# Performance work log

Hardware: AMD Instinct MI355X
Metric: run time of the kernel (lower is better)

The kernel has to match this reference:

```python
import jax, jax.numpy as jnp
import numpy as np

N_NODES = 100000
N_EDGES = 1600000
F_IN = 128
HID = 128  # nhid*2
NHID = 64
N_GRAPHS = 512
N_CLASSES = 10
NEG_SLOPE = 0.2  # PyG GATConv default


def setup_inputs() -> dict:
    key = jax.random.key(0)
    ks = jax.random.split(key, 16)
    x = jax.random.normal(ks[0], (N_NODES, F_IN), dtype=jnp.float32)
    edge_index = jax.random.randint(ks[1], (2, N_EDGES), 0, N_NODES, dtype=jnp.int64)
    batch = jnp.sort(jax.random.randint(ks[2], (N_NODES,), 0, N_GRAPHS, dtype=jnp.int64))
    def lin(k, fan_in, shape):
        bound = 1.0 / np.sqrt(fan_in)
        return jax.random.uniform(k, shape, jnp.float32, -bound, bound)
    return {
        "x": x, "edge_index": edge_index, "batch": batch,
        "W1": lin(ks[3], F_IN, (F_IN, HID)),
        "a_src1": lin(ks[4], HID, (HID,)),
        "a_dst1": lin(ks[5], HID, (HID,)),
        "b1": jnp.zeros((HID,), jnp.float32),
        "W2": lin(ks[6], HID, (HID, HID)),
        "a_src2": lin(ks[7], HID, (HID,)),
        "a_dst2": lin(ks[8], HID, (HID,)),
        "b2": jnp.zeros((HID,), jnp.float32),
        "W_fc1": lin(ks[9], HID, (HID, NHID)),
        "b_fc1": lin(ks[10], HID, (NHID,)),
        "W_fc2": lin(ks[11], NHID, (NHID, N_CLASSES)),
        "b_fc2": lin(ks[12], NHID, (N_CLASSES,)),
    }


def gat_conv(x, src, dst, W, a_src, a_dst, b):
    # h = W x ; attention e_ij = LeakyReLU(a_src.h_i + a_dst.h_j), softmax over
    # incoming edges of each destination j, then scatter-add aggregation.
    h = x @ W                                   # [N, H]
    alpha_s = h @ a_src                         # [N]
    alpha_d = h @ a_dst                         # [N]
    e = jax.nn.leaky_relu(alpha_s[src] + alpha_d[dst], NEG_SLOPE)  # [E]
    n = x.shape[0]
    m = jax.ops.segment_max(e, dst, num_segments=n)                # per-dst max
    ex = jnp.exp(e - m[dst])
    denom = jax.ops.segment_sum(ex, dst, num_segments=n)
    alpha = ex / denom[dst]                                        # [E]
    out = jax.ops.segment_sum(alpha[:, None] * h[src], dst, num_segments=n)
    return out + b


def reference(x, edge_index, batch, W1, a_src1, a_dst1, b1,
              W2, a_src2, a_dst2, b2, W_fc1, b_fc1, W_fc2, b_fc2):
    n = x.shape[0]
    # GATConv default add_self_loops=True
    loops = jnp.arange(n, dtype=edge_index.dtype)
    src = jnp.concatenate([edge_index[0], loops])
    dst = jnp.concatenate([edge_index[1], loops])

    h = jax.nn.selu(gat_conv(x, src, dst, W1, a_src1, a_dst1, b1))
    h = jax.nn.selu(gat_conv(h, src, dst, W2, a_src2, a_dst2, b2))

    # global mean pool over graphs
    sums = jax.ops.segment_sum(h, batch, num_segments=N_GRAPHS)
    cnts = jax.ops.segment_sum(jnp.ones((n,), h.dtype), batch, num_segments=N_GRAPHS)
    pooled = jax.nn.selu(sums / jnp.maximum(cnts, 1.0)[:, None])   # [G, H]

    g = jax.nn.selu(pooled @ W_fc1 + b_fc1)
    # dropout p=0.5 is identity in eval mode
    logits = g @ W_fc2 + b_fc2
    return jax.nn.log_softmax(logits, axis=-1)
```

## Files before the change

kernel.cpp:

```cpp
#include <hip/hip_runtime.h>
#include <hip/hip_bf16.h>

#define NEG_SLOPE 0.2f
typedef unsigned int uint32;

#define BSHIFT 9
#define BSIZE 512
#define MAXB 256
#define PCHUNK 4096

typedef __attribute__((ext_vector_type(8))) __bf16 bf16x8;
typedef __attribute__((ext_vector_type(4))) float f32x4;

__device__ __forceinline__ float selu_f(float x) {
    const float a = 1.6732632423543772f, s = 1.0507009873554805f;
    return x > 0.0f ? s * x : s * a * (__expf(x) - 1.0f);
}

__device__ __forceinline__ unsigned short f2bf(float x) {
    uint32 u = __float_as_uint(x);
    uint32 r = (u + 0x7fff + ((u >> 16) & 1)) >> 16;
    return (unsigned short)r;
}
__device__ __forceinline__ float bf_lo(uint32 g) { return __uint_as_float(g << 16); }
__device__ __forceinline__ float bf_hi(uint32 g) { return __uint_as_float(g & 0xffff0000u); }

__global__ __launch_bounds__(256) void repack_w(const float* __restrict__ W1,
                                                const float* __restrict__ W2,
                                                unsigned short* __restrict__ Wb) {
    const float* W = blockIdx.x ? W2 : W1;
    unsigned short* oh = Wb + (size_t)blockIdx.x * 32768;
    unsigned short* ol = oh + 16384;
    for (int d = threadIdx.x; d < 16384; d += 256) {
        int j = d & 7, nn = (d >> 3) & 127, g = d >> 10;
        float v = W[(g * 8 + j) * 128 + nn];
        uint32 hu = f2bf(v);
        float hv = __uint_as_float(hu << 16);
        oh[d] = (unsigned short)hu;
        ol[d] = f2bf(v - hv);
    }
}

__device__ __forceinline__ void gemm_core(const bf16x8 ah[2][4],
                                          const __bf16* Wl,
                                          const float* a_src, const float* a_dst,
                                          uint32* hb, float* as_, float* ad_,
                                          int rbase, int n, int col16, int quad) {
    f32x4 acc[2][8];
    #pragma unroll
    for (int mt = 0; mt < 2; ++mt)
        #pragma unroll
        for (int t = 0; t < 8; ++t) acc[mt][t] = (f32x4)(0.0f);

    #pragma unroll
    for (int c = 0; c < 4; ++c) {
        #pragma unroll
        for (int t = 0; t < 8; ++t) {
            int off = (((c * 4 + quad) * 128) + t * 16 + col16) * 8;
            bf16x8 bh = *(const bf16x8*)&Wl[off];
            bf16x8 bl = *(const bf16x8*)&Wl[16384 + off];
            #pragma unroll
            for (int mt = 0; mt < 2; ++mt) {
                acc[mt][t] = __builtin_amdgcn_mfma_f32_16x16x32_bf16(ah[mt][c], bh, acc[mt][t], 0, 0, 0);
                acc[mt][t] = __builtin_amdgcn_mfma_f32_16x16x32_bf16(ah[mt][c], bl, acc[mt][t], 0, 0, 0);
            }
        }
    }
    float asv[8], adv[8];
    #pragma unroll
    for (int t = 0; t < 8; ++t) { asv[t] = a_src[t * 16 + col16]; adv[t] = a_dst[t * 16 + col16]; }
    #pragma unroll
    for (int mt = 0; mt < 2; ++mt) {
        #pragma unroll
        for (int reg = 0; reg < 4; ++reg) {
            float s = 0.0f, d = 0.0f;
            #pragma unroll
            for (int t = 0; t < 8; ++t) {
                float v = acc[mt][t][reg];
                s += v * asv[t]; d += v * adv[t];
            }
            #pragma unroll
            for (int off = 1; off < 16; off <<= 1) {
                s += __shfl_xor(s, off);
                d += __shfl_xor(d, off);
            }
            int r = rbase + mt * 16 + quad * 4 + reg;
            if (col16 == 0 && r < n) { as_[r] = s; ad_[r] = d; }
        }
    }
    #pragma unroll
    for (int mt = 0; mt < 2; ++mt)
    #pragma unroll
    for (int t = 0; t < 8; ++t)
    #pragma unroll
    for (int reg = 0; reg < 4; ++reg) {
        float v = acc[mt][t][reg];
        float p = __shfl_xor(v, 1);
        int r = rbase + mt * 16 + quad * 4 + reg;
        if (!(col16 & 1) && r < n) {
            uint32 pk = (uint32)f2bf(v) | ((uint32)f2bf(p) << 16);
            hb[(size_t)r * 64 + t * 8 + (col16 >> 1)] = pk;
        }
    }
}

__global__ __launch_bounds__(256) void gemm_mfma_f32(const float* __restrict__ X,
                                                     const unsigned short* __restrict__ Wbh,
                                                     const float* __restrict__ a_src,
                                                     const float* __restrict__ a_dst,
                                                     uint32* __restrict__ hb,
                                                     float* __restrict__ as_,
                                                     float* __restrict__ ad_, int n) {
    __shared__ __bf16 Wl[32768];
    const int tid = threadIdx.x;
    {
        const uint4* sw = (const uint4*)Wbh;
        uint4* dw = (uint4*)Wl;
        for (int i = tid; i < 4096; i += 256) dw[i] = sw[i];
    }
    const int lane = tid & 63, wid = tid >> 6;
    const int col16 = lane & 15, quad = lane >> 4;
    const int rbase = blockIdx.x * 128 + wid * 32;
    bf16x8 ah[2][4];
    #pragma unroll
    for (int mt = 0; mt < 2; ++mt) {
        int r = rbase + mt * 16 + col16;
        bool ok = (r < n);
        const float* xp = X + (size_t)r * 128;
        #pragma unroll
        for (int c = 0; c < 4; ++c) {
            int k0 = c * 32 + quad * 8;
            float4 x0 = ok ? *(const float4*)(xp + k0)     : make_float4(0.f,0.f,0.f,0.f);
            float4 x1 = ok ? *(const float4*)(xp + k0 + 4) : make_float4(0.f,0.f,0.f,0.f);
            float xs[8] = {x0.x,x0.y,x0.z,x0.w,x1.x,x1.y,x1.z,x1.w};
            #pragma unroll
            for (int j = 0; j < 8; ++j) ah[mt][c][j] = (__bf16)xs[j];
        }
    }
    __syncthreads();
    gemm_core(ah, Wl, a_src, a_dst, hb, as_, ad_, rbase, n, col16, quad);
}

__global__ __launch_bounds__(256) void gemm_mfma_bf16(const __bf16* __restrict__ X,
                                                      const unsigned short* __restrict__ Wbh,
                                                      const float* __restrict__ a_src,
                                                      const float* __restrict__ a_dst,
                                                      uint32* __restrict__ hb,
                                                      float* __restrict__ as_,
                                                      float* __restrict__ ad_, int n) {
    __shared__ __bf16 Wl[32768];
    const int tid = threadIdx.x;
    {
        const uint4* sw = (const uint4*)Wbh;
        uint4* dw = (uint4*)Wl;
        for (int i = tid; i < 4096; i += 256) dw[i] = sw[i];
    }
    const int lane = tid & 63, wid = tid >> 6;
    const int col16 = lane & 15, quad = lane >> 4;
    const int rbase = blockIdx.x * 128 + wid * 32;
    bf16x8 ah[2][4];
    const bf16x8 zz = (bf16x8)((__bf16)0.0f);
    #pragma unroll
    for (int mt = 0; mt < 2; ++mt) {
        int r = rbase + mt * 16 + col16;
        bool ok = (r < n);
        const __bf16* xp = X + (size_t)r * 128;
        #pragma unroll
        for (int c = 0; c < 4; ++c)
            ah[mt][c] = ok ? *(const bf16x8*)(xp + c * 32 + quad * 8) : zz;
    }
    __syncthreads();
    gemm_core(ah, Wl, a_src, a_dst, hb, as_, ad_, rbase, n, col16, quad);
}

__global__ __launch_bounds__(256) void bucket_hist(const int* __restrict__ ei,
                                                   int* __restrict__ gcnt, int E, int TOT) {
    __shared__ int lh[MAXB];
    int t = threadIdx.x;
    lh[t] = 0;
    __syncthreads();
    int eb = blockIdx.x * PCHUNK;
    #pragma unroll
    for (int k = 0; k < PCHUNK / 256; ++k) {
        int e = eb + k * 256 + t;
        if (e < TOT) {
            int d = (e < E) ? ei[E + e] : e - E;
            atomicAdd(&lh[d >> BSHIFT], 1);
        }
    }
    __syncthreads();
    if (lh[t] > 0) atomicAdd(&gcnt[t], lh[t]);
}

__global__ __launch_bounds__(256) void bucket_scan(const int* __restrict__ gcnt,
                                                   int* __restrict__ bstart,
                                                   int* __restrict__ gcursor, int NB, int TOT) {
    __shared__ int sh[256];
    int t = threadIdx.x;
    int v = (t < NB) ? gcnt[t] : 0;
    sh[t] = v;
    __syncthreads();
    for (int off = 1; off < 256; off <<= 1) {
        int add = (t >= off) ? sh[t - off] : 0;
        __syncthreads();
        sh[t] += add;
        __syncthreads();
    }
    int ex = sh[t] - v;
    if (t < NB) { bstart[t] = ex; gcursor[t] = ex; }
    if (t == 0) bstart[NB] = TOT;
}

__global__ __launch_bounds__(256) void partition_edges(const int* __restrict__ ei,
                                                       int* __restrict__ gcursor,
                                                       uint32* __restrict__ tmp,
                                                       int E, int TOT) {
    __shared__ int lcnt[MAXB];
    __shared__ int lstart[MAXB];
    __shared__ int lcur[MAXB];
    __shared__ int gbase[MAXB];
    __shared__ uint32 staged[PCHUNK];
    __shared__ unsigned char bslot[PCHUNK];
    int t = threadIdx.x;
    int eb = blockIdx.x * PCHUNK;
    int sreg[16], dreg[16];
    #pragma unroll
    for (int k = 0; k < 16; ++k) {
        int e = eb + k * 256 + t;
        if (e < TOT) {
            if (e < E) { sreg[k] = ei[e]; dreg[k] = ei[E + e]; }
            else       { sreg[k] = dreg[k] = e - E; }
        } else dreg[k] = -1;
    }
    lcnt[t] = 0;
    __syncthreads();
    #pragma unroll
    for (int k = 0; k < 16; ++k)
        if (dreg[k] >= 0) atomicAdd(&lcnt[dreg[k] >> BSHIFT], 1);
    __syncthreads();
    int v = lcnt[t];
    lstart[t] = v;
    __syncthreads();
    for (int off = 1; off < 256; off <<= 1) {
        int add = (t >= off) ? lstart[t - off] : 0;
        __syncthreads();
        lstart[t] += add;
        __syncthreads();
    }
    int ex = lstart[t] - v;
    __syncthreads();
    lstart[t] = ex;
    lcur[t] = ex;
    if (v > 0) gbase[t] = atomicAdd(&gcursor[t], v);
    __syncthreads();
    #pragma unroll
    for (int k = 0; k < 16; ++k) {
        int d = dreg[k];
        if (d >= 0) {
            int b = d >> BSHIFT;
            int p = atomicAdd(&lcur[b], 1);
            staged[p] = ((uint32)(d & (BSIZE - 1)) << 17) | (uint32)sreg[k];
            bslot[p] = (unsigned char)b;
        }
    }
    __syncthreads();
    int nvalid = TOT - eb; if (nvalid > PCHUNK) nvalid = PCHUNK;
    for (int i = t; i < nvalid; i += 256) {
        int b = bslot[i];
        tmp[gbase[b] + (i - lstart[b])] = staged[i];
    }
}

__global__ __launch_bounds__(256) void bucket_build(const uint32* __restrict__ tmp,
                                                    const int* __restrict__ bstart,
                                                    int* __restrict__ rowptr,
                                                    int* __restrict__ col,
                                                    int N, int TOT, int NB) {
    __shared__ int cnt[BSIZE];
    __shared__ int sums[256];
    int b = blockIdx.x, t = threadIdx.x;
    int lo = b << BSHIFT;
    int nn = N - lo; if (nn > BSIZE) nn = BSIZE;
    cnt[t] = 0; cnt[t + 256] = 0;
    __syncthreads();
    int ebeg = bstart[b], eend = bstart[b + 1];
    for (int i = ebeg + t; i < eend; i += 256)
        atomicAdd(&cnt[tmp[i] >> 17], 1);
    __syncthreads();
    int c0 = cnt[2 * t], c1 = cnt[2 * t + 1];
    int s2 = c0 + c1;
    sums[t] = s2;
    __syncthreads();
    for (int off = 1; off < 256; off <<= 1) {
        int add = (t >= off) ? sums[t - off] : 0;
        __syncthreads();
        sums[t] += add;
        __syncthreads();
    }
    int ex = sums[t] - s2;
    int st0 = ebeg + ex, st1 = st0 + c0;
    if (2 * t < nn)     rowptr[lo + 2 * t] = st0;
    if (2 * t + 1 < nn) rowptr[lo + 2 * t + 1] = st1;
    cnt[2 * t] = st0; cnt[2 * t + 1] = st1;
    __syncthreads();
    for (int i = ebeg + t; i < eend; i += 256) {
        uint32 u = tmp[i];
        int p = atomicAdd(&cnt[u >> 17], 1);
        col[p] = (int)(u & 0x1FFFFu);
    }
    if (b == NB - 1 && t == 0) rowptr[N] = TOT;
}

__global__ __launch_bounds__(256) void gat_csr3(const int* __restrict__ rowptr,
                                                const int* __restrict__ col,
                                                const uint2* __restrict__ hb2,
                                                const float* __restrict__ as_,
                                                const float* __restrict__ ad_,
                                                const float* __restrict__ bias,
                                                uint2* __restrict__ outb, int n) {
    __shared__ float wsh[4][2][32];
    __shared__ int   ssh[4][2][32];
    const int wid = threadIdx.x >> 6;
    const int lane = threadIdx.x & 63;
    const int sub = lane >> 5, l = lane & 31;
    const int node = blockIdx.x * 8 + wid * 2 + sub;
    const bool valid = node < n;
    int beg = 0, end = 0;
    if (valid) { beg = rowptr[node]; end = rowptr[node + 1]; }
    float add = valid ? ad_[node] : 0.0f;
    int deg = end - beg;
    int mdeg = max(deg, __shfl_xor(deg, 32));
    float m = -INFINITY, s = 0.0f;
    float a0 = 0.f, a1 = 0.f, a2 = 0.f, a3 = 0.f;
    for (int cb = 0; cb < mdeg; cb += 32) {
        int j = beg + cb + l;
        bool eok = (j < end);
        int srcn = eok ? col[j] : 0;
        float v = eok ? (as_[srcn] + add) : -INFINITY;
        v = (v > 0.0f) ? v : NEG_SLOPE * v;
        float cm = v;
        #pragma unroll
        for (int off = 16; off > 0; off >>= 1) cm = fmaxf(cm, __shfl_xor(cm, off));
        float nm = fmaxf(m, cm);
        float w = eok ? __expf(v - nm) : 0.0f;
        float ws = w;
        #pragma unroll
        for (int off = 16; off > 0; off >>= 1) ws += __shfl_xor(ws, off);
        float scale = (m == -INFINITY) ? 0.0f : __expf(m - nm);
        s = s * scale + ws;
        a0 *= scale; a1 *= scale; a2 *= scale; a3 *= scale;
        wsh[wid][sub][l] = w;
        ssh[wid][sub][l] = srcn;
        int cnt = end - beg - cb;
        cnt = (cnt > 32) ? 32 : (cnt < 0 ? 0 : cnt);
        int t = 0;
        for (; t + 8 <= cnt; t += 8) {
            int sr[8]; float wr[8]; uint2 g[8];
            #pragma unroll
            for (int q = 0; q < 8; ++q) { sr[q] = ssh[wid][sub][t + q]; wr[q] = wsh[wid][sub][t + q]; }
            #pragma unroll
            for (int q = 0; q < 8; ++q) g[q] = hb2[(uint32)sr[q] * 32u + l];
            #pragma unroll
            for (int q = 0; q < 8; ++q) {
                a0 += wr[q] * bf_lo(g[q].x); a1 += wr[q] * bf_hi(g[q].x);
                a2 += wr[q] * bf_lo(g[q].y); a3 += wr[q] * bf_hi(g[q].y);
            }
        }
        for (; t < cnt; ++t) {
            int sn = ssh[wid][sub][t];
            float wt = wsh[wid][sub][t];
            uint2 g = hb2[(uint32)sn * 32u + l];
            a0 += wt * bf_lo(g.x); a1 += wt * bf_hi(g.x);
            a2 += wt * bf_lo(g.y); a3 += wt * bf_hi(g.y);
        }
        m = nm;
    }
    if (valid) {
        float inv = 1.0f / s;
        float4 bv = *(const float4*)&bias[l * 4];
        float r0 = selu_f(a0 * inv + bv.x);
        float r1 = selu_f(a1 * inv + bv.y);
        float r2 = selu_f(a2 * inv + bv.z);
        float r3 = selu_f(a3 * inv + bv.w);
        uint2 o;
        o.x = (uint32)f2bf(r0) | ((uint32)f2bf(r1) << 16);
        o.y = (uint32)f2bf(r2) | ((uint32)f2bf(r3) << 16);
        outb[(uint32)node * 32u + l] = o;
    }
}

__global__ __launch_bounds__(256) void graph_bounds(const int* __restrict__ batch,
                                                    int* __restrict__ gstart, int n, int G) {
    int i = blockIdx.x * 256 + threadIdx.x;
    if (i >= n) return;
    int b = batch[i];
    int bp = (i == 0) ? -1 : batch[i - 1];
    for (int q = bp + 1; q <= b; ++q) gstart[q] = i;
    if (i == n - 1)
        for (int q = b + 1; q <= G; ++q) gstart[q] = n;
}

__global__ __launch_bounds__(128) void pool_head(const uint32* __restrict__ act,
                                                 const int* __restrict__ gstart,
                                                 const float* __restrict__ Wfc1,
                                                 const float* __restrict__ bfc1,
                                                 const float* __restrict__ Wfc2,
                                                 const float* __restrict__ bfc2,
                                                 float* __restrict__ out) {
    __shared__ float part[128][2];
    __shared__ float p[128];
    __shared__ float q[64];
    __shared__ float l[10];
    __shared__ float red[2];
    int g = blockIdx.x, t = threadIdx.x;
    int lo = gstart[g], hi = gstart[g + 1];
    int half = t >> 6, u = t & 63;
    float acc0 = 0.f, acc1 = 0.f;
    for (int nd = lo + half; nd < hi; nd += 2) {
        uint32 gv = act[(uint32)nd * 64u + u];
        acc0 += bf_lo(gv); acc1 += bf_hi(gv);
    }
    part[t][0] = acc0; part[t][1] = acc1;
    __syncthreads();
    if (half == 0) {
        float c = fmaxf((float)(hi - lo), 1.0f);
        p[2 * u]     = selu_f((acc0 + part[t + 64][0]) / c);
        p[2 * u + 1] = selu_f((acc1 + part[t + 64][1]) / c);
    }
    __syncthreads();
    if (t < 64) {
        float a = bfc1[t];
        #pragma unroll 8
        for (int k = 0; k < 128; ++k) a += p[k] * Wfc1[k * 64 + t];
        q[t] = selu_f(a);
    }
    __syncthreads();
    if (t < 10) {
        float a = bfc2[t];
        #pragma unroll
        for (int k = 0; k < 64; ++k) a += q[k] * Wfc2[k * 10 + t];
        l[t] = a;
    }
    __syncthreads();
    if (t == 0) {
        float mx = l[0];
        for (int c = 1; c < 10; ++c) mx = fmaxf(mx, l[c]);
        float sum = 0.0f;
        for (int c = 0; c < 10; ++c) sum += __expf(l[c] - mx);
        red[0] = mx; red[1] = logf(sum);
    }
    __syncthreads();
    if (t < 10) out[g * 10 + t] = l[t] - red[0] - red[1];
}

extern "C" void kernel_launch(void* const* d_in, const int* in_sizes, int n_in,
                              void* d_out, int out_size, void* d_ws, size_t ws_size,
                              hipStream_t stream) {
    const float* x      = (const float*)d_in[0];
    const int*   ei     = (const int*)d_in[1];
    const int*   batch  = (const int*)d_in[2];
    const float* W1     = (const float*)d_in[3];
    const float* asrc1  = (const float*)d_in[4];
    const float* adst1  = (const float*)d_in[5];
    const float* b1     = (const float*)d_in[6];
    const float* W2     = (const float*)d_in[7];
    const float* asrc2  = (const float*)d_in[8];
    const float* adst2  = (const float*)d_in[9];
    const float* b2     = (const float*)d_in[10];
    const float* Wfc1   = (const float*)d_in[11];
    const float* bfc1   = (const float*)d_in[12];
    const float* Wfc2   = (const float*)d_in[13];
    const float* bfc2   = (const float*)d_in[14];
    float* out = (float*)d_out;

    const int N = in_sizes[0] / 128;
    const int E = in_sizes[1] / 2;
    const int G = out_size / 10;
    const int TOT = E + N;
    const int NB = ((N - 1) >> BSHIFT) + 1;

    uint32* hb    = (uint32*)d_ws;
    uint32* h2b   = hb + (size_t)N * 64;
    uint32* tmp   = h2b + (size_t)N * 64;
    float* as_    = (float*)(tmp + TOT);
    float* ad_    = as_ + N;
    int*   gstart = (int*)(ad_ + N);
    int*   rowptr = gstart + (G + 2);
    int*   gcnt   = rowptr + (N + 2);
    int*   bstart = gcnt + MAXB;
    int*   gcursor= bstart + MAXB + 1;
    int*   col    = gcursor + MAXB;
    unsigned short* Wb = (unsigned short*)(((uintptr_t)(col + TOT) + 255) & ~(uintptr_t)255);

    const int gemmGrid = (N + 127) / 128;
    const int partGrid = (TOT + PCHUNK - 1) / PCHUNK;
    const int gatGrid  = (N + 7) / 8;

    repack_w<<<2, 256, 0, stream>>>(W1, W2, Wb);
    hipMemsetAsync(gcnt, 0, MAXB * 4, stream);
    bucket_hist<<<partGrid, 256, 0, stream>>>(ei, gcnt, E, TOT);
    bucket_scan<<<1, 256, 0, stream>>>(gcnt, bstart, gcursor, NB, TOT);
    partition_edges<<<partGrid, 256, 0, stream>>>(ei, gcursor, tmp, E, TOT);
    bucket_build<<<NB, 256, 0, stream>>>(tmp, bstart, rowptr, col, N, TOT, NB);
    graph_bounds<<<(N + 255) / 256, 256, 0, stream>>>(batch, gstart, N, G);

    gemm_mfma_f32<<<gemmGrid, 256, 0, stream>>>(x, Wb, asrc1, adst1, hb, as_, ad_, N);
    gat_csr3<<<gatGrid, 256, 0, stream>>>(rowptr, col, (const uint2*)hb, as_, ad_, b1, (uint2*)h2b, N);

    gemm_mfma_bf16<<<gemmGrid, 256, 0, stream>>>((const __bf16*)h2b, Wb + 32768, asrc2, adst2, hb, as_, ad_, N);
    gat_csr3<<<gatGrid, 256, 0, stream>>>(rowptr, col, (const uint2*)hb, as_, ad_, b2, (uint2*)h2b, N);

    pool_head<<<G, 128, 0, stream>>>(h2b, gstart, Wfc1, bfc1, Wfc2, bfc2, out);
}
```

Before: 417.8 us.

## Fuse setup kernels and switch GAT aggregation to one wave per node

```diff
diff --git a/kernel.cpp b/kernel.cpp
--- a/kernel.cpp
+++ b/kernel.cpp
@@ -25,20 +25,175 @@
 __device__ __forceinline__ float bf_lo(uint32 g) { return __uint_as_float(g << 16); }
 __device__ __forceinline__ float bf_hi(uint32 g) { return __uint_as_float(g & 0xffff0000u); }
 
-__global__ __launch_bounds__(256) void repack_w(const float* __restrict__ W1,
-                                                const float* __restrict__ W2,
-                                                unsigned short* __restrict__ Wb) {
-    const float* W = blockIdx.x ? W2 : W1;
-    unsigned short* oh = Wb + (size_t)blockIdx.x * 32768;
-    unsigned short* ol = oh + 16384;
-    for (int d = threadIdx.x; d < 16384; d += 256) {
-        int j = d & 7, nn = (d >> 3) & 127, g = d >> 10;
-        float v = W[(g * 8 + j) * 128 + nn];
-        uint32 hu = f2bf(v);
-        float hv = __uint_as_float(hu << 16);
-        oh[d] = (unsigned short)hu;
-        ol[d] = f2bf(v - hv);
-    }
+__global__ __launch_bounds__(256) void prep(const float* __restrict__ W1,
+                                            const float* __restrict__ W2,
+                                            unsigned short* __restrict__ Wb,
+                                            const int* __restrict__ batch,
+                                            int* __restrict__ gstart,
+                                            const int* __restrict__ ei,
+                                            int* __restrict__ gpart,
+                                            int N, int G, int E, int TOT, int GB) {
+    __shared__ int lh[MAXB];
+    int b = blockIdx.x, t = threadIdx.x;
+    if (b < 2) {
+        const float* W = b ? W2 : W1;
+        unsigned short* oh = Wb + (size_t)b * 32768;
+        unsigned short* ol = oh + 16384;
+        for (int d = t; d < 16384; d += 256) {
+            int j = d & 7, nn = (d >> 3) & 127, g = d >> 10;
+            float v = W[(g * 8 + j) * 128 + nn];
+            uint32 hu = f2bf(v);
+            float hv = __uint_as_float(hu << 16);
+            oh[d] = (unsigned short)hu;
+            ol[d] = f2bf(v - hv);
+        }
+    } else if (b < 2 + GB) {
+        int i = (b - 2) * 256 + t;
+        if (i < N) {
+            int bb = batch[i];
+            int bp = (i == 0) ? -1 : batch[i - 1];
+            for (int q = bp + 1; q <= bb; ++q) gstart[q] = i;
+            if (i == N - 1)
+                for (int q = bb + 1; q <= G; ++q) gstart[q] = N;
+        }
+    } else {
+        int hb_ = b - 2 - GB;
+        lh[t] = 0;
+        __syncthreads();
+        int eb = hb_ * PCHUNK;
+        #pragma unroll
+        for (int k = 0; k < PCHUNK / 256; ++k) {
+            int e = eb + k * 256 + t;
+            if (e < TOT) {
+                int d = (e < E) ? ei[E + e] : e - E;
+                atomicAdd(&lh[d >> BSHIFT], 1);
+            }
+        }
+        __syncthreads();
+        gpart[hb_ * MAXB + t] = lh[t];
+    }
+}
+
+__global__ __launch_bounds__(256) void bucket_scan2(const int* __restrict__ gpart,
+                                                    int nparts,
+                                                    int* __restrict__ bstart,
+                                                    int* __restrict__ gcursor,
+                                                    int NB, int TOT) {
+    __shared__ int sh[256];
+    int t = threadIdx.x;
+    int v = 0;
+    for (int p = 0; p < nparts; ++p) v += gpart[p * MAXB + t];
+    sh[t] = v;
+    __syncthreads();
+    for (int off = 1; off < 256; off <<= 1) {
+        int add = (t >= off) ? sh[t - off] : 0;
+        __syncthreads();
+        sh[t] += add;
+        __syncthreads();
+    }
+    int ex = sh[t] - v;
+    if (t < NB) { bstart[t] = ex; gcursor[t] = ex; }
+    if (t == 0) bstart[NB] = TOT;
+}
+
+__global__ __launch_bounds__(256) void partition_edges(const int* __restrict__ ei,
+                                                       int* __restrict__ gcursor,
+                                                       uint32* __restrict__ tmp,
+                                                       int E, int TOT) {
+    __shared__ int lcnt[MAXB];
+    __shared__ int lstart[MAXB];
+    __shared__ int lcur[MAXB];
+    __shared__ int gbase[MAXB];
+    __shared__ uint32 staged[PCHUNK];
+    __shared__ unsigned char bslot[PCHUNK];
+    int t = threadIdx.x;
+    int eb = blockIdx.x * PCHUNK;
+    int sreg[16], dreg[16];
+    #pragma unroll
+    for (int k = 0; k < 16; ++k) {
+        int e = eb + k * 256 + t;
+        if (e < TOT) {
+            if (e < E) { sreg[k] = ei[e]; dreg[k] = ei[E + e]; }
+            else       { sreg[k] = dreg[k] = e - E; }
+        } else dreg[k] = -1;
+    }
+    lcnt[t] = 0;
+    __syncthreads();
+    #pragma unroll
+    for (int k = 0; k < 16; ++k)
+        if (dreg[k] >= 0) atomicAdd(&lcnt[dreg[k] >> BSHIFT], 1);
+    __syncthreads();
+    int v = lcnt[t];
+    lstart[t] = v;
+    __syncthreads();
+    for (int off = 1; off < 256; off <<= 1) {
+        int add = (t >= off) ? lstart[t - off] : 0;
+        __syncthreads();
+        lstart[t] += add;
+        __syncthreads();
+    }
+    int ex = lstart[t] - v;
+    __syncthreads();
+    lstart[t] = ex;
+    lcur[t] = ex;
+    if (v > 0) gbase[t] = atomicAdd(&gcursor[t], v);
+    __syncthreads();
+    #pragma unroll
+    for (int k = 0; k < 16; ++k) {
+        int d = dreg[k];
+        if (d >= 0) {
+            int b = d >> BSHIFT;
+            int p = atomicAdd(&lcur[b], 1);
+            staged[p] = ((uint32)(d & (BSIZE - 1)) << 17) | (uint32)sreg[k];
+            bslot[p] = (unsigned char)b;
+        }
+    }
+    __syncthreads();
+    int nvalid = TOT - eb; if (nvalid > PCHUNK) nvalid = PCHUNK;
+    for (int i = t; i < nvalid; i += 256) {
+        int b = bslot[i];
+        tmp[gbase[b] + (i - lstart[b])] = staged[i];
+    }
+}
+
+__global__ __launch_bounds__(256) void bucket_build(const uint32* __restrict__ tmp,
+                                                    const int* __restrict__ bstart,
+                                                    int* __restrict__ rowptr,
+                                                    int* __restrict__ col,
+                                                    int N, int TOT, int NB) {
+    __shared__ int cnt[BSIZE];
+    __shared__ int sums[256];
+    int b = blockIdx.x, t = threadIdx.x;
+    int lo = b << BSHIFT;
+    int nn = N - lo; if (nn > BSIZE) nn = BSIZE;
+    cnt[t] = 0; cnt[t + 256] = 0;
+    __syncthreads();
+    int ebeg = bstart[b], eend = bstart[b + 1];
+    for (int i = ebeg + t; i < eend; i += 256)
+        atomicAdd(&cnt[tmp[i] >> 17], 1);
+    __syncthreads();
+    int c0 = cnt[2 * t], c1 = cnt[2 * t + 1];
+    int s2 = c0 + c1;
+    sums[t] = s2;
+    __syncthreads();
+    for (int off = 1; off < 256; off <<= 1) {
+        int add = (t >= off) ? sums[t - off] : 0;
+        __syncthreads();
+        sums[t] += add;
+        __syncthreads();
+    }
+    int ex = sums[t] - s2;
+    int st0 = ebeg + ex, st1 = st0 + c0;
+    if (2 * t < nn)     rowptr[lo + 2 * t] = st0;
+    if (2 * t + 1 < nn) rowptr[lo + 2 * t + 1] = st1;
+    cnt[2 * t] = st0; cnt[2 * t + 1] = st1;
+    __syncthreads();
+    for (int i = ebeg + t; i < eend; i += 256) {
+        uint32 u = tmp[i];
+        int p = atomicAdd(&cnt[u >> 17], 1);
+        col[p] = (int)(u & 0x1FFFFu);
+    }
+    if (b == NB - 1 && t == 0) rowptr[N] = TOT;
 }
 
 __device__ __forceinline__ void gemm_core(const bf16x8 ah[2][4],
@@ -173,231 +328,93 @@
     gemm_core(ah, Wl, a_src, a_dst, hb, as_, ad_, rbase, n, col16, quad);
 }
 
-__global__ __launch_bounds__(256) void bucket_hist(const int* __restrict__ ei,
-                                                   int* __restrict__ gcnt, int E, int TOT) {
-    __shared__ int lh[MAXB];
-    int t = threadIdx.x;
-    lh[t] = 0;
-    __syncthreads();
-    int eb = blockIdx.x * PCHUNK;
-    #pragma unroll
-    for (int k = 0; k < PCHUNK / 256; ++k) {
-        int e = eb + k * 256 + t;
-        if (e < TOT) {
-            int d = (e < E) ? ei[E + e] : e - E;
-            atomicAdd(&lh[d >> BSHIFT], 1);
-        }
-    }
-    __syncthreads();
-    if (lh[t] > 0) atomicAdd(&gcnt[t], lh[t]);
-}
-
-__global__ __launch_bounds__(256) void bucket_scan(const int* __restrict__ gcnt,
-                                                   int* __restrict__ bstart,
-                                                   int* __restrict__ gcursor, int NB, int TOT) {
-    __shared__ int sh[256];
-    int t = threadIdx.x;
-    int v = (t < NB) ? gcnt[t] : 0;
-    sh[t] = v;
-    __syncthreads();
-    for (int off = 1; off < 256; off <<= 1) {
-        int add = (t >= off) ? sh[t - off] : 0;
-        __syncthreads();
-        sh[t] += add;
-        __syncthreads();
-    }
-    int ex = sh[t] - v;
-    if (t < NB) { bstart[t] = ex; gcursor[t] = ex; }
-    if (t == 0) bstart[NB] = TOT;
-}
-
-__global__ __launch_bounds__(256) void partition_edges(const int* __restrict__ ei,
-                                                       int* __restrict__ gcursor,
-                                                       uint32* __restrict__ tmp,
-                                                       int E, int TOT) {
-    __shared__ int lcnt[MAXB];
-    __shared__ int lstart[MAXB];
-    __shared__ int lcur[MAXB];
-    __shared__ int gbase[MAXB];
-    __shared__ uint32 staged[PCHUNK];
-    __shared__ unsigned char bslot[PCHUNK];
-    int t = threadIdx.x;
-    int eb = blockIdx.x * PCHUNK;
-    int sreg[16], dreg[16];
-    #pragma unroll
-    for (int k = 0; k < 16; ++k) {
-        int e = eb + k * 256 + t;
-        if (e < TOT) {
-            if (e < E) { sreg[k] = ei[e]; dreg[k] = ei[E + e]; }
-            else       { sreg[k] = dreg[k] = e - E; }
-        } else dreg[k] = -1;
-    }
-    lcnt[t] = 0;
-    __syncthreads();
-    #pragma unroll
-    for (int k = 0; k < 16; ++k)
-        if (dreg[k] >= 0) atomicAdd(&lcnt[dreg[k] >> BSHIFT], 1);
-    __syncthreads();
-    int v = lcnt[t];
-    lstart[t] = v;
-    __syncthreads();
-    for (int off = 1; off < 256; off <<= 1) {
-        int add = (t >= off) ? lstart[t - off] : 0;
-        __syncthreads();
-        lstart[t] += add;
-        __syncthreads();
-    }
-    int ex = lstart[t] - v;
-    __syncthreads();
-    lstart[t] = ex;
-    lcur[t] = ex;
-    if (v > 0) gbase[t] = atomicAdd(&gcursor[t], v);
-    __syncthreads();
-    #pragma unroll
-    for (int k = 0; k < 16; ++k) {
-        int d = dreg[k];
-        if (d >= 0) {
-            int b = d >> BSHIFT;
-            int p = atomicAdd(&lcur[b], 1);
-            staged[p] = ((uint32)(d & (BSIZE - 1)) << 17) | (uint32)sreg[k];
-            bslot[p] = (unsigned char)b;
-        }
-    }
-    __syncthreads();
-    int nvalid = TOT - eb; if (nvalid > PCHUNK) nvalid = PCHUNK;
-    for (int i = t; i < nvalid; i += 256) {
-        int b = bslot[i];
-        tmp[gbase[b] + (i - lstart[b])] = staged[i];
-    }
-}
-
-__global__ __launch_bounds__(256) void bucket_build(const uint32* __restrict__ tmp,
-                                                    const int* __restrict__ bstart,
-                                                    int* __restrict__ rowptr,
-                                                    int* __restrict__ col,
-                                                    int N, int TOT, int NB) {
-    __shared__ int cnt[BSIZE];
-    __shared__ int sums[256];
-    int b = blockIdx.x, t = threadIdx.x;
-    int lo = b << BSHIFT;
-    int nn = N - lo; if (nn > BSIZE) nn = BSIZE;
-    cnt[t] = 0; cnt[t + 256] = 0;
-    __syncthreads();
-    int ebeg = bstart[b], eend = bstart[b + 1];
-    for (int i = ebeg + t; i < eend; i += 256)
-        atomicAdd(&cnt[tmp[i] >> 17], 1);
-    __syncthreads();
-    int c0 = cnt[2 * t], c1 = cnt[2 * t + 1];
-    int s2 = c0 + c1;
-    sums[t] = s2;
-    __syncthreads();
-    for (int off = 1; off < 256; off <<= 1) {
-        int add = (t >= off) ? sums[t - off] : 0;
-        __syncthreads();
-        sums[t] += add;
-        __syncthreads();
-    }
-    int ex = sums[t] - s2;
-    int st0 = ebeg + ex, st1 = st0 + c0;
-    if (2 * t < nn)     rowptr[lo + 2 * t] = st0;
-    if (2 * t + 1 < nn) rowptr[lo + 2 * t + 1] = st1;
-    cnt[2 * t] = st0; cnt[2 * t + 1] = st1;
-    __syncthreads();
-    for (int i = ebeg + t; i < eend; i += 256) {
-        uint32 u = tmp[i];
-        int p = atomicAdd(&cnt[u >> 17], 1);
-        col[p] = (int)(u & 0x1FFFFu);
-    }
-    if (b == NB - 1 && t == 0) rowptr[N] = TOT;
-}
-
-__global__ __launch_bounds__(256) void gat_csr3(const int* __restrict__ rowptr,
+__global__ __launch_bounds__(256) void gat_csr4(const int* __restrict__ rowptr,
                                                 const int* __restrict__ col,
-                                                const uint2* __restrict__ hb2,
+                                                const uint4* __restrict__ hb4,
                                                 const float* __restrict__ as_,
                                                 const float* __restrict__ ad_,
                                                 const float* __restrict__ bias,
-                                                uint2* __restrict__ outb, int n) {
-    __shared__ float wsh[4][2][32];
-    __shared__ int   ssh[4][2][32];
+                                                uint4* __restrict__ outb4, int n) {
     const int wid = threadIdx.x >> 6;
     const int lane = threadIdx.x & 63;
-    const int sub = lane >> 5, l = lane & 31;
-    const int node = blockIdx.x * 8 + wid * 2 + sub;
-    const bool valid = node < n;
-    int beg = 0, end = 0;
-    if (valid) { beg = rowptr[node]; end = rowptr[node + 1]; }
-    float add = valid ? ad_[node] : 0.0f;
-    int deg = end - beg;
-    int mdeg = max(deg, __shfl_xor(deg, 32));
+    const int grp = lane >> 4, fl = lane & 15;
+    const int node = blockIdx.x * 4 + wid;
+    if (node >= n) return;
+    const int beg = rowptr[node], end = rowptr[node + 1];
+    const float add = ad_[node];
+    const int deg = end - beg;
     float m = -INFINITY, s = 0.0f;
-    float a0 = 0.f, a1 = 0.f, a2 = 0.f, a3 = 0.f;
-    for (int cb = 0; cb < mdeg; cb += 32) {
-        int j = beg + cb + l;
+    float a0=0.f,a1=0.f,a2=0.f,a3=0.f,a4=0.f,a5=0.f,a6=0.f,a7=0.f;
+    for (int cb = 0; cb < deg; cb += 64) {
+        int j = beg + cb + lane;
         bool eok = (j < end);
         int srcn = eok ? col[j] : 0;
         float v = eok ? (as_[srcn] + add) : -INFINITY;
         v = (v > 0.0f) ? v : NEG_SLOPE * v;
         float cm = v;
         #pragma unroll
-        for (int off = 16; off > 0; off >>= 1) cm = fmaxf(cm, __shfl_xor(cm, off));
+        for (int off = 32; off > 0; off >>= 1) cm = fmaxf(cm, __shfl_xor(cm, off));
         float nm = fmaxf(m, cm);
         float w = eok ? __expf(v - nm) : 0.0f;
         float ws = w;
         #pragma unroll
-        for (int off = 16; off > 0; off >>= 1) ws += __shfl_xor(ws, off);
+        for (int off = 32; off > 0; off >>= 1) ws += __shfl_xor(ws, off);
         float scale = (m == -INFINITY) ? 0.0f : __expf(m - nm);
         s = s * scale + ws;
-        a0 *= scale; a1 *= scale; a2 *= scale; a3 *= scale;
-        wsh[wid][sub][l] = w;
-        ssh[wid][sub][l] = srcn;
-        int cnt = end - beg - cb;
-        cnt = (cnt > 32) ? 32 : (cnt < 0 ? 0 : cnt);
-        int t = 0;
-        for (; t + 8 <= cnt; t += 8) {
-            int sr[8]; float wr[8]; uint2 g[8];
-            #pragma unroll
-            for (int q = 0; q < 8; ++q) { sr[q] = ssh[wid][sub][t + q]; wr[q] = wsh[wid][sub][t + q]; }
-            #pragma unroll
-            for (int q = 0; q < 8; ++q) g[q] = hb2[(uint32)sr[q] * 32u + l];
-            #pragma unroll
-            for (int q = 0; q < 8; ++q) {
-                a0 += wr[q] * bf_lo(g[q].x); a1 += wr[q] * bf_hi(g[q].x);
-                a2 += wr[q] * bf_lo(g[q].y); a3 += wr[q] * bf_hi(g[q].y);
+        a0*=scale; a1*=scale; a2*=scale; a3*=scale;
+        a4*=scale; a5*=scale; a6*=scale; a7*=scale;
+        int cnt = end - beg - cb; cnt = (cnt > 64) ? 64 : cnt;
+        for (int tt = 0; tt < cnt; tt += 8) {
+            int e0 = tt + grp, e1 = tt + 4 + grp;
+            float w0 = __shfl(w, e0);
+            int   s0 = __shfl(srcn, e0);
+            float w1 = __shfl(w, e1);
+            int   s1 = __shfl(srcn, e1);
+            bool v0 = e0 < cnt, v1 = e1 < cnt;
+            uint4 g0, g1;
+            if (v0) g0 = hb4[(uint32)s0 * 16u + fl];
+            if (v1) g1 = hb4[(uint32)s1 * 16u + fl];
+            if (v0) {
+                a0 += w0 * bf_lo(g0.x); a1 += w0 * bf_hi(g0.x);
+                a2 += w0 * bf_lo(g0.y); a3 += w0 * bf_hi(g0.y);
+                a4 += w0 * bf_lo(g0.z); a5 += w0 * bf_hi(g0.z);
+                a6 += w0 * bf_lo(g0.w); a7 += w0 * bf_hi(g0.w);
             }
-        }
-        for (; t < cnt; ++t) {
-            int sn = ssh[wid][sub][t];
-            float wt = wsh[wid][sub][t];
-            uint2 g = hb2[(uint32)sn * 32u + l];
-            a0 += wt * bf_lo(g.x); a1 += wt * bf_hi(g.x);
-            a2 += wt * bf_lo(g.y); a3 += wt * bf_hi(g.y);
+            if (v1) {
+                a0 += w1 * bf_lo(g1.x); a1 += w1 * bf_hi(g1.x);
+                a2 += w1 * bf_lo(g1.y); a3 += w1 * bf_hi(g1.y);
+                a4 += w1 * bf_lo(g1.z); a5 += w1 * bf_hi(g1.z);
+                a6 += w1 * bf_lo(g1.w); a7 += w1 * bf_hi(g1.w);
+            }
         }
         m = nm;
     }
-    if (valid) {
+    #pragma unroll
+    for (int off = 16; off < 64; off <<= 1) {
+        a0 += __shfl_xor(a0, off); a1 += __shfl_xor(a1, off);
+        a2 += __shfl_xor(a2, off); a3 += __shfl_xor(a3, off);
+        a4 += __shfl_xor(a4, off); a5 += __shfl_xor(a5, off);
+        a6 += __shfl_xor(a6, off); a7 += __shfl_xor(a7, off);
+    }
+    if (grp == 0) {
         float inv = 1.0f / s;
-        float4 bv = *(const float4*)&bias[l * 4];
-        float r0 = selu_f(a0 * inv + bv.x);
-        float r1 = selu_f(a1 * inv + bv.y);
-        float r2 = selu_f(a2 * inv + bv.z);
-        float r3 = selu_f(a3 * inv + bv.w);
-        uint2 o;
+        float4 b0 = *(const float4*)&bias[fl * 8];
+        float4 b1 = *(const float4*)&bias[fl * 8 + 4];
+        float r0 = selu_f(a0 * inv + b0.x);
+        float r1 = selu_f(a1 * inv + b0.y);
+        float r2 = selu_f(a2 * inv + b0.z);
+        float r3 = selu_f(a3 * inv + b0.w);
+        float r4 = selu_f(a4 * inv + b1.x);
+        float r5 = selu_f(a5 * inv + b1.y);
+        float r6 = selu_f(a6 * inv + b1.z);
+        float r7 = selu_f(a7 * inv + b1.w);
+        uint4 o;
         o.x = (uint32)f2bf(r0) | ((uint32)f2bf(r1) << 16);
         o.y = (uint32)f2bf(r2) | ((uint32)f2bf(r3) << 16);
-        outb[(uint32)node * 32u + l] = o;
-    }
-}
-
-__global__ __launch_bounds__(256) void graph_bounds(const int* __restrict__ batch,
-                                                    int* __restrict__ gstart, int n, int G) {
-    int i = blockIdx.x * 256 + threadIdx.x;
-    if (i >= n) return;
-    int b = batch[i];
-    int bp = (i == 0) ? -1 : batch[i - 1];
-    for (int q = bp + 1; q <= b; ++q) gstart[q] = i;
-    if (i == n - 1)
-        for (int q = b + 1; q <= G; ++q) gstart[q] = n;
+        o.z = (uint32)f2bf(r4) | ((uint32)f2bf(r5) << 16);
+        o.w = (uint32)f2bf(r6) | ((uint32)f2bf(r7) << 16);
+        outb4[(uint32)node * 16u + fl] = o;
+    }
 }
 
 __global__ __launch_bounds__(128) void pool_head(const uint32* __restrict__ act,
@@ -478,6 +495,8 @@
     const int G = out_size / 10;
     const int TOT = E + N;
     const int NB = ((N - 1) >> BSHIFT) + 1;
+    const int GB = (N + 255) / 256;
+    const int PH = (TOT + PCHUNK - 1) / PCHUNK;
 
     uint32* hb    = (uint32*)d_ws;
     uint32* h2b   = hb + (size_t)N * 64;
@@ -486,29 +505,25 @@
     float* ad_    = as_ + N;
     int*   gstart = (int*)(ad_ + N);
     int*   rowptr = gstart + (G + 2);
-    int*   gcnt   = rowptr + (N + 2);
-    int*   bstart = gcnt + MAXB;
+    int*   bstart = rowptr + (N + 2);
     int*   gcursor= bstart + MAXB + 1;
-    int*   col    = gcursor + MAXB;
+    int*   gpart  = gcursor + MAXB;
+    int*   col    = gpart + PH * MAXB;
     unsigned short* Wb = (unsigned short*)(((uintptr_t)(col + TOT) + 255) & ~(uintptr_t)255);
 
     const int gemmGrid = (N + 127) / 128;
-    const int partGrid = (TOT + PCHUNK - 1) / PCHUNK;
-    const int gatGrid  = (N + 7) / 8;
-
-    repack_w<<<2, 256, 0, stream>>>(W1, W2, Wb);
-    hipMemsetAsync(gcnt, 0, MAXB * 4, stream);
-    bucket_hist<<<partGrid, 256, 0, stream>>>(ei, gcnt, E, TOT);
-    bucket_scan<<<1, 256, 0, stream>>>(gcnt, bstart, gcursor, NB, TOT);
-    partition_edges<<<partGrid, 256, 0, stream>>>(ei, gcursor, tmp, E, TOT);
+    const int gatGrid  = (N + 3) / 4;
+
+    prep<<<2 + GB + PH, 256, 0, stream>>>(W1, W2, Wb, batch, gstart, ei, gpart, N, G, E, TOT, GB);
+    bucket_scan2<<<1, 256, 0, stream>>>(gpart, PH, bstart, gcursor, NB, TOT);
+    partition_edges<<<PH, 256, 0, stream>>>(ei, gcursor, tmp, E, TOT);
     bucket_build<<<NB, 256, 0, stream>>>(tmp, bstart, rowptr, col, N, TOT, NB);
-    graph_bounds<<<(N + 255) / 256, 256, 0, stream>>>(batch, gstart, N, G);
 
     gemm_mfma_f32<<<gemmGrid, 256, 0, stream>>>(x, Wb, asrc1, adst1, hb, as_, ad_, N);
-    gat_csr3<<<gatGrid, 256, 0, stream>>>(rowptr, col, (const uint2*)hb, as_, ad_, b1, (uint2*)h2b, N);
+    gat_csr4<<<gatGrid, 256, 0, stream>>>(rowptr, col, (const uint4*)hb, as_, ad_, b1, (uint4*)h2b, N);
 
     gemm_mfma_bf16<<<gemmGrid, 256, 0, stream>>>((const __bf16*)h2b, Wb + 32768, asrc2, adst2, hb, as_, ad_, N);
-    gat_csr3<<<gatGrid, 256, 0, stream>>>(rowptr, col, (const uint2*)hb, as_, ad_, b2, (uint2*)h2b, N);
+    gat_csr4<<<gatGrid, 256, 0, stream>>>(rowptr, col, (const uint4*)hb, as_, ad_, b2, (uint4*)h2b, N);
 
     pool_head<<<G, 128, 0, stream>>>(h2b, gstart, Wfc1, bfc1, Wfc2, bfc2, out);
 }
```

Measured after the change: 468.2 us. 12.1% more time.

## Merge CSR preprocessing into fused prep kernel with per-chunk local partitions

Applied to the files above, without the earlier changes.

```diff
diff --git a/kernel.cpp b/kernel.cpp
--- a/kernel.cpp
+++ b/kernel.cpp
@@ -25,20 +25,160 @@
 __device__ __forceinline__ float bf_lo(uint32 g) { return __uint_as_float(g << 16); }
 __device__ __forceinline__ float bf_hi(uint32 g) { return __uint_as_float(g & 0xffff0000u); }
 
-__global__ __launch_bounds__(256) void repack_w(const float* __restrict__ W1,
-                                                const float* __restrict__ W2,
-                                                unsigned short* __restrict__ Wb) {
-    const float* W = blockIdx.x ? W2 : W1;
-    unsigned short* oh = Wb + (size_t)blockIdx.x * 32768;
-    unsigned short* ol = oh + 16384;
-    for (int d = threadIdx.x; d < 16384; d += 256) {
-        int j = d & 7, nn = (d >> 3) & 127, g = d >> 10;
-        float v = W[(g * 8 + j) * 128 + nn];
-        uint32 hu = f2bf(v);
-        float hv = __uint_as_float(hu << 16);
-        oh[d] = (unsigned short)hu;
-        ol[d] = f2bf(v - hv);
-    }
+__global__ __launch_bounds__(256) void prep(const float* __restrict__ W1,
+                                            const float* __restrict__ W2,
+                                            unsigned short* __restrict__ Wb,
+                                            const int* __restrict__ batch,
+                                            int* __restrict__ gstart,
+                                            const int* __restrict__ ei,
+                                            uint32* __restrict__ tmp,
+                                            int* __restrict__ cntp,
+                                            int* __restrict__ offp,
+                                            int N, int G, int E, int TOT, int GB) {
+    __shared__ uint32 staged[PCHUNK];
+    __shared__ int lcnt[MAXB];
+    __shared__ int lstart[MAXB];
+    __shared__ int lcur[MAXB];
+    int b = blockIdx.x, t = threadIdx.x;
+    if (b < 2) {
+        const float* W = b ? W2 : W1;
+        unsigned short* oh = Wb + (size_t)b * 32768;
+        unsigned short* ol = oh + 16384;
+        for (int d = t; d < 16384; d += 256) {
+            int j = d & 7, nn = (d >> 3) & 127, g = d >> 10;
+            float v = W[(g * 8 + j) * 128 + nn];
+            uint32 hu = f2bf(v);
+            float hv = __uint_as_float(hu << 16);
+            oh[d] = (unsigned short)hu;
+            ol[d] = f2bf(v - hv);
+        }
+    } else if (b < 2 + GB) {
+        int i = (b - 2) * 256 + t;
+        if (i < N) {
+            int bb = batch[i];
+            int bp = (i == 0) ? -1 : batch[i - 1];
+            for (int q = bp + 1; q <= bb; ++q) gstart[q] = i;
+            if (i == N - 1)
+                for (int q = bb + 1; q <= G; ++q) gstart[q] = N;
+        }
+    } else {
+        int c = b - 2 - GB;
+        int eb = c * PCHUNK;
+        int sreg[16], dreg[16];
+        #pragma unroll
+        for (int k = 0; k < 16; ++k) {
+            int e = eb + k * 256 + t;
+            if (e < TOT) {
+                if (e < E) { sreg[k] = ei[e]; dreg[k] = ei[E + e]; }
+                else       { sreg[k] = dreg[k] = e - E; }
+            } else dreg[k] = -1;
+        }
+        lcnt[t] = 0;
+        __syncthreads();
+        #pragma unroll
+        for (int k = 0; k < 16; ++k)
+            if (dreg[k] >= 0) atomicAdd(&lcnt[dreg[k] >> BSHIFT], 1);
+        __syncthreads();
+        int v = lcnt[t];
+        lstart[t] = v;
+        __syncthreads();
+        for (int off = 1; off < 256; off <<= 1) {
+            int add = (t >= off) ? lstart[t - off] : 0;
+            __syncthreads();
+            lstart[t] += add;
+            __syncthreads();
+        }
+        int ex = lstart[t] - v;
+        cntp[c * MAXB + t] = v;
+        offp[c * MAXB + t] = ex;
+        __syncthreads();
+        lstart[t] = ex;
+        lcur[t] = ex;
+        __syncthreads();
+        #pragma unroll
+        for (int k = 0; k < 16; ++k) {
+            int d = dreg[k];
+            if (d >= 0) {
+                int p = atomicAdd(&lcur[d >> BSHIFT], 1);
+                staged[p] = ((uint32)(d & (BSIZE - 1)) << 17) | (uint32)sreg[k];
+            }
+        }
+        __syncthreads();
+        int nvalid = TOT - eb; if (nvalid > PCHUNK) nvalid = PCHUNK;
+        for (int i = t; i < nvalid; i += 256)
+            tmp[eb + i] = staged[i];
+    }
+}
+
+__global__ __launch_bounds__(256) void scan3(const int* __restrict__ cntp,
+                                             int nchunks,
+                                             int* __restrict__ bstart,
+                                             int NB, int TOT) {
+    __shared__ int sh[256];
+    int t = threadIdx.x;
+    int v = 0;
+    for (int c = 0; c < nchunks; ++c) v += cntp[c * MAXB + t];
+    sh[t] = v;
+    __syncthreads();
+    for (int off = 1; off < 256; off <<= 1) {
+        int add = (t >= off) ? sh[t - off] : 0;
+        __syncthreads();
+        sh[t] += add;
+        __syncthreads();
+    }
+    int ex = sh[t] - v;
+    if (t < NB) bstart[t] = ex;
+    if (t == 0) bstart[NB] = TOT;
+}
+
+__global__ __launch_bounds__(256) void bucket_build2(const uint32* __restrict__ tmp,
+                                                     const int* __restrict__ cntp,
+                                                     const int* __restrict__ offp,
+                                                     const int* __restrict__ bstart,
+                                                     int* __restrict__ rowptr,
+                                                     int* __restrict__ col,
+                                                     int N, int TOT, int NB, int PH) {
+    __shared__ int cnt[BSIZE];
+    __shared__ int sums[256];
+    int b = blockIdx.x, t = threadIdx.x;
+    int lo = b << BSHIFT;
+    int nn = N - lo; if (nn > BSIZE) nn = BSIZE;
+    cnt[t] = 0; cnt[t + 256] = 0;
+    __syncthreads();
+    for (int c = t; c < PH; c += 256) {
+        int cc = cntp[c * MAXB + b];
+        int oo = c * PCHUNK + offp[c * MAXB + b];
+        for (int i = 0; i < cc; ++i)
+            atomicAdd(&cnt[tmp[oo + i] >> 17], 1);
+    }
+    __syncthreads();
+    int c0 = cnt[2 * t], c1 = cnt[2 * t + 1];
+    int s2 = c0 + c1;
+    sums[t] = s2;
+    __syncthreads();
+    for (int off = 1; off < 256; off <<= 1) {
+        int add = (t >= off) ? sums[t - off] : 0;
+        __syncthreads();
+        sums[t] += add;
+        __syncthreads();
+    }
+    int ebeg = bstart[b];
+    int ex = sums[t] - s2;
+    int st0 = ebeg + ex, st1 = st0 + c0;
+    if (2 * t < nn)     rowptr[lo + 2 * t] = st0;
+    if (2 * t + 1 < nn) rowptr[lo + 2 * t + 1] = st1;
+    cnt[2 * t] = st0; cnt[2 * t + 1] = st1;
+    __syncthreads();
+    for (int c = t; c < PH; c += 256) {
+        int cc = cntp[c * MAXB + b];
+        int oo = c * PCHUNK + offp[c * MAXB + b];
+        for (int i = 0; i < cc; ++i) {
+            uint32 u = tmp[oo + i];
+            int p = atomicAdd(&cnt[u >> 17], 1);
+            col[p] = (int)(u & 0x1FFFFu);
+        }
+    }
+    if (b == NB - 1 && t == 0) rowptr[N] = TOT;
 }
 
 __device__ __forceinline__ void gemm_core(const bf16x8 ah[2][4],
@@ -171,144 +311,6 @@
     }
     __syncthreads();
     gemm_core(ah, Wl, a_src, a_dst, hb, as_, ad_, rbase, n, col16, quad);
-}
-
-__global__ __launch_bounds__(256) void bucket_hist(const int* __restrict__ ei,
-                                                   int* __restrict__ gcnt, int E, int TOT) {
-    __shared__ int lh[MAXB];
-    int t = threadIdx.x;
-    lh[t] = 0;
-    __syncthreads();
-    int eb = blockIdx.x * PCHUNK;
-    #pragma unroll
-    for (int k = 0; k < PCHUNK / 256; ++k) {
-        int e = eb + k * 256 + t;
-        if (e < TOT) {
-            int d = (e < E) ? ei[E + e] : e - E;
-            atomicAdd(&lh[d >> BSHIFT], 1);
-        }
-    }
-    __syncthreads();
-    if (lh[t] > 0) atomicAdd(&gcnt[t], lh[t]);
-}
-
-__global__ __launch_bounds__(256) void bucket_scan(const int* __restrict__ gcnt,
-                                                   int* __restrict__ bstart,
-                                                   int* __restrict__ gcursor, int NB, int TOT) {
-    __shared__ int sh[256];
-    int t = threadIdx.x;
-    int v = (t < NB) ? gcnt[t] : 0;
-    sh[t] = v;
-    __syncthreads();
-    for (int off = 1; off < 256; off <<= 1) {
-        int add = (t >= off) ? sh[t - off] : 0;
-        __syncthreads();
-        sh[t] += add;
-        __syncthreads();
-    }
-    int ex = sh[t] - v;
-    if (t < NB) { bstart[t] = ex; gcursor[t] = ex; }
-    if (t == 0) bstart[NB] = TOT;
-}
-
-__global__ __launch_bounds__(256) void partition_edges(const int* __restrict__ ei,
-                                                       int* __restrict__ gcursor,
-                                                       uint32* __restrict__ tmp,
-                                                       int E, int TOT) {
-    __shared__ int lcnt[MAXB];
-    __shared__ int lstart[MAXB];
-    __shared__ int lcur[MAXB];
-    __shared__ int gbase[MAXB];
-    __shared__ uint32 staged[PCHUNK];
-    __shared__ unsigned char bslot[PCHUNK];
-    int t = threadIdx.x;
-    int eb = blockIdx.x * PCHUNK;
-    int sreg[16], dreg[16];
-    #pragma unroll
-    for (int k = 0; k < 16; ++k) {
-        int e = eb + k * 256 + t;
-        if (e < TOT) {
-            if (e < E) { sreg[k] = ei[e]; dreg[k] = ei[E + e]; }
-            else       { sreg[k] = dreg[k] = e - E; }
-        } else dreg[k] = -1;
-    }
-    lcnt[t] = 0;
-    __syncthreads();
-    #pragma unroll
-    for (int k = 0; k < 16; ++k)
-        if (dreg[k] >= 0) atomicAdd(&lcnt[dreg[k] >> BSHIFT], 1);
-    __syncthreads();
-    int v = lcnt[t];
-    lstart[t] = v;
-    __syncthreads();
-    for (int off = 1; off < 256; off <<= 1) {
-        int add = (t >= off) ? lstart[t - off] : 0;
-        __syncthreads();
-        lstart[t] += add;
-        __syncthreads();
-    }
-    int ex = lstart[t] - v;
-    __syncthreads();
-    lstart[t] = ex;
-    lcur[t] = ex;
-    if (v > 0) gbase[t] = atomicAdd(&gcursor[t], v);
-    __syncthreads();
-    #pragma unroll
-    for (int k = 0; k < 16; ++k) {
-        int d = dreg[k];
-        if (d >= 0) {
-            int b = d >> BSHIFT;
-            int p = atomicAdd(&lcur[b], 1);
-            staged[p] = ((uint32)(d & (BSIZE - 1)) << 17) | (uint32)sreg[k];
-            bslot[p] = (unsigned char)b;
-        }
-    }
-    __syncthreads();
-    int nvalid = TOT - eb; if (nvalid > PCHUNK) nvalid = PCHUNK;
-    for (int i = t; i < nvalid; i += 256) {
-        int b = bslot[i];
-        tmp[gbase[b] + (i - lstart[b])] = staged[i];
-    }
-}
-
-__global__ __launch_bounds__(256) void bucket_build(const uint32* __restrict__ tmp,
-                                                    const int* __restrict__ bstart,
-                                                    int* __restrict__ rowptr,
-                                                    int* __restrict__ col,
-                                                    int N, int TOT, int NB) {
-    __shared__ int cnt[BSIZE];
-    __shared__ int sums[256];
-    int b = blockIdx.x, t = threadIdx.x;
-    int lo = b << BSHIFT;
-    int nn = N - lo; if (nn > BSIZE) nn = BSIZE;
-    cnt[t] = 0; cnt[t + 256] = 0;
-    __syncthreads();
-    int ebeg = bstart[b], eend = bstart[b + 1];
-    for (int i = ebeg + t; i < eend; i += 256)
-        atomicAdd(&cnt[tmp[i] >> 17], 1);
-    __syncthreads();
-    int c0 = cnt[2 * t], c1 = cnt[2 * t + 1];
-    int s2 = c0 + c1;
-    sums[t] = s2;
-    __syncthreads();
-    for (int off = 1; off < 256; off <<= 1) {
-        int add = (t >= off) ? sums[t - off] : 0;
-        __syncthreads();
-        sums[t] += add;
-        __syncthreads();
-    }
-    int ex = sums[t] - s2;
-    int st0 = ebeg + ex, st1 = st0 + c0;
-    if (2 * t < nn)     rowptr[lo + 2 * t] = st0;
-    if (2 * t + 1 < nn) rowptr[lo + 2 * t + 1] = st1;
-    cnt[2 * t] = st0; cnt[2 * t + 1] = st1;
-    __syncthreads();
-    for (int i = ebeg + t; i < eend; i += 256) {
-        uint32 u = tmp[i];
-        int p = atomicAdd(&cnt[u >> 17], 1);
-        col[p] = (int)(u & 0x1FFFFu);
-    }
-    if (b == NB - 1 && t == 0) rowptr[N] = TOT;
 }
 
 __global__ __launch_bounds__(256) void gat_csr3(const int* __restrict__ rowptr,
@@ -389,17 +391,6 @@
     }
 }
 
-__global__ __launch_bounds__(256) void graph_bounds(const int* __restrict__ batch,
-                                                    int* __restrict__ gstart, int n, int G) {
-    int i = blockIdx.x * 256 + threadIdx.x;
-    if (i >= n) return;
-    int b = batch[i];
-    int bp = (i == 0) ? -1 : batch[i - 1];
-    for (int q = bp + 1; q <= b; ++q) gstart[q] = i;
-    if (i == n - 1)
-        for (int q = b + 1; q <= G; ++q) gstart[q] = n;
-}
-
 __global__ __launch_bounds__(128) void pool_head(const uint32* __restrict__ act,
                                                  const int* __restrict__ gstart,
                                                  const float* __restrict__ Wfc1,
@@ -478,31 +469,30 @@
     const int G = out_size / 10;
     const int TOT = E + N;
     const int NB = ((N - 1) >> BSHIFT) + 1;
+    const int GB = (N + 255) / 256;
+    const int PH = (TOT + PCHUNK - 1) / PCHUNK;
 
     uint32* hb    = (uint32*)d_ws;
     uint32* h2b   = hb + (size_t)N * 64;
     uint32* tmp   = h2b + (size_t)N * 64;
-    float* as_    = (float*)(tmp + TOT);
+    float* as_    = (float*)(tmp + (size_t)PH * PCHUNK);
     float* ad_    = as_ + N;
     int*   gstart = (int*)(ad_ + N);
     int*   rowptr = gstart + (G + 2);
-    int*   gcnt   = rowptr + (N + 2);
-    int*   bstart = gcnt + MAXB;
-    int*   gcursor= bstart + MAXB + 1;
-    int*   col    = gcursor + MAXB;
+    int*   bstart = rowptr + (N + 2);
+    int*   cntp   = bstart + MAXB + 1;
+    int*   offp   = cntp + PH * MAXB;
+    int*   col    = offp + PH * MAXB;
     unsigned short* Wb = (unsigned short*)(((uintptr_t)(col + TOT) + 255) & ~(uintptr_t)255);
 
     const int gemmGrid = (N + 127) / 128;
-    const int partGrid = (TOT + PCHUNK - 1) / PCHUNK;
     const int gatGrid  = (N + 7) / 8;
 
-    repack_w<<<2, 256, 0, stream>>>(W1, W2, Wb);
-    hipMemsetAsync(gcnt, 0, MAXB * 4, stream);
-    bucket_hist<<<partGrid, 256, 0, stream>>>(ei, gcnt, E, TOT);
-    bucket_scan<<<1, 256, 0, stream>>>(gcnt, bstart, gcursor, NB, TOT);
-    partition_edges<<<partGrid, 256, 0, stream>>>(ei, gcursor, tmp, E, TOT);
-    bucket_build<<<NB, 256, 0, stream>>>(tmp, bstart, rowptr, col, N, TOT, NB);
-    graph_bounds<<<(N + 255) / 256, 256, 0, stream>>>(batch, gstart, N, G);
+    prep<<<2 + GB + PH, 256, 0, stream>>>(W1, W2, Wb, batch, gstart, ei, tmp,
+                                          cntp, offp, N, G, E, TOT, GB);
+    scan3<<<1, 256, 0, stream>>>(cntp, PH, bstart, NB, TOT);
+    bucket_build2<<<NB, 256, 0, stream>>>(tmp, cntp, offp, bstart, rowptr, col,
+                                          N, TOT, NB, PH);
 
     gemm_mfma_f32<<<gemmGrid, 256, 0, stream>>>(x, Wb, asrc1, adst1, hb, as_, ad_, N);
     gat_csr3<<<gatGrid, 256, 0, stream>>>(rowptr, col, (const uint2*)hb, as_, ad_, b1, (uint2*)h2b, N);
```

Measured after the change: 469.9 us. +12.5%, slower.
